# Optimization experiments

Hardware: AMD Instinct MI355X
Metric: run time of the kernel (lower is better)

Reference implementation:

```python
import jax, jax.numpy as jnp
import numpy as np

NEG_INF = -1e9
LRELU_SLOPE = 0.2  # torch GAT default leaky_relu negative slope


def setup_inputs() -> dict:
    key = jax.random.key(0)
    k1, k2, k3, k4, k5 = jax.random.split(key, 5)
    N, F_IN, H, DH = 4096, 1433, 8, 8  # n_nodes, in_features, n_heads, per-head dim (n_hidden=64)
    vert = jax.random.normal(k1, (N, F_IN), dtype=jnp.float32)
    edge = jax.random.randint(k2, (N, N), 0, 2, dtype=jnp.int32)  # dense adjacency mask
    W = jax.random.normal(k3, (F_IN, H * DH), dtype=jnp.float32) * 0.05
    a_l = jax.random.normal(k4, (H, DH), dtype=jnp.float32) * 0.05
    a_r = jax.random.normal(k5, (H, DH), dtype=jnp.float32) * 0.05
    return {"vert": vert, "edge": edge, "W": W, "a_l": a_l, "a_r": a_r}


def reference(vert, edge, W, a_l, a_r):
    # GAT-style edge-affinity layer (is_concat=True) + ELU; dropout is identity (eval mode).
    N = vert.shape[0]
    H, DH = a_l.shape
    g = (vert @ W).reshape(N, H, DH)                      # [N,H,Dh] projected node features
    sl = jnp.einsum('nhd,hd->nh', g, a_l)                 # source-node attention term
    sr = jnp.einsum('nhd,hd->nh', g, a_r)                 # target-node attention term
    e = sl[:, None, :] + sr[None, :, :]                   # [N,N,H]: attn([g_i || g_j])
    e = jnp.where(e >= 0, e, LRELU_SLOPE * e)             # leaky_relu
    mask = (edge != 0)[:, :, None]                        # [N,N,1]
    e = jnp.where(mask, e, NEG_INF)                       # mask non-edges
    a = jax.nn.softmax(e, axis=1)                         # normalize over neighbors j
    out = jnp.einsum('ijh,jhd->ihd', a, g).reshape(N, H * DH)  # aggregate + concat heads
    return jax.nn.elu(out)
```

## Files before the change

kernel.cpp:

```cpp
#include <hip/hip_runtime.h>
#include <hip/hip_bf16.h>

#define NN 4096
#define FIN 1433
#define NH 8
#define DH 8
#define HD 64
#define KP 1472
#define LOG2E 1.44269504f
#define NJS 8
#define ITB 32
#define NCHK ((NN / NJS) / 64)
#define NKS 4

typedef unsigned int u32;
typedef unsigned long long u64;
typedef float v4f __attribute__((ext_vector_type(4)));
typedef _Float16 f16;
typedef _Float16 h2 __attribute__((ext_vector_type(2)));
typedef _Float16 f16x8 __attribute__((ext_vector_type(8)));

static __device__ __forceinline__ short f2h16(float f) {
    union { f16 h; short s; } u; u.h = (f16)f; return u.s;
}
static __device__ __forceinline__ h2 u2h2(u32 x) {
    union { u32 u; h2 h; } v; v.u = x; return v.h;
}
static __device__ __forceinline__ u32 h22u(h2 x) {
    union { h2 h; u32 u; } v; v.h = x; return v.u;
}

#if __has_builtin(__builtin_amdgcn_sbfe)
#define SBFE1(x, k) __builtin_amdgcn_sbfe((int)(x), (k), 1)
#else
#define SBFE1(x, k) (((int)((x) << (31 - (k)))) >> 31)
#endif

static __device__ __forceinline__ void gload_lds16(const void* g, void* l) {
    __builtin_amdgcn_global_load_lds(
        (const __attribute__((address_space(1))) void*)g,
        (__attribute__((address_space(3))) void*)l, 16, 0, 0);
}

__global__ __launch_bounds__(256) void k_wprep(const float* __restrict__ W,
                                               short* __restrict__ Wt) {
    __shared__ float Ts[64][65];
    const int c = blockIdx.x;
    const int u = threadIdx.x;
    const int n4 = (u & 15) * 4;
    const int kr = u >> 4;
#pragma unroll
    for (int q = 0; q < 4; ++q) {
        const int kl = kr + q * 16;
        const int kg = c * 64 + kl;
        v4f v = {0.f, 0.f, 0.f, 0.f};
        if (kg < FIN) v = *(const v4f*)&W[(size_t)kg * HD + n4];
        *(v4f*)&Ts[kl][n4] = v;
    }
    __syncthreads();
    const int n = u >> 2;
    const int koff = (u & 3) * 16;
    __align__(16) short tmp[16];
#pragma unroll
    for (int r = 0; r < 16; ++r) tmp[r] = f2h16(Ts[koff + r][n]);
    *(uint4*)&Wt[(size_t)n * KP + c * 64 + koff]     = *(uint4*)&tmp[0];
    *(uint4*)&Wt[(size_t)n * KP + c * 64 + koff + 8] = *(uint4*)&tmp[8];
}

__global__ __launch_bounds__(256, 4) void k_gemm(
    const float* __restrict__ vert, const short* __restrict__ Wt,
    float* __restrict__ Cp)
{
    __shared__ float cacc[4][16][68];

    const int t = threadIdx.x, lane = t & 63, w = t >> 6;
    const int ml = lane & 15, q = lane >> 4;
    const int i0 = blockIdx.x * 16;
    const int ks = blockIdx.y;
    const float* vrow = vert + (size_t)(i0 + ml) * FIN;

    v4f acc[4];
#pragma unroll
    for (int g = 0; g < 4; ++g) acc[g] = (v4f){0.f, 0.f, 0.f, 0.f};

    for (int c = ks + 4 * w; c < 45; c += 16) {
        const int k0 = c * 32 + q * 8;
        v4f a0, a1;
        if (k0 + 7 < FIN) {
            a0 = *(const v4f*)&vrow[k0];
            a1 = *(const v4f*)&vrow[k0 + 4];
        } else {
            float tmp[8];
#pragma unroll
            for (int e = 0; e < 8; ++e)
                tmp[e] = (k0 + e < FIN) ? vrow[k0 + e] : 0.f;
            a0 = (v4f){tmp[0], tmp[1], tmp[2], tmp[3]};
            a1 = (v4f){tmp[4], tmp[5], tmp[6], tmp[7]};
        }
        const f16x8 af = {(f16)a0.x, (f16)a0.y, (f16)a0.z, (f16)a0.w,
                          (f16)a1.x, (f16)a1.y, (f16)a1.z, (f16)a1.w};
#pragma unroll
        for (int g = 0; g < 4; ++g) {
            const f16x8 bf = *(const f16x8*)&Wt[(size_t)(g * 16 + ml) * KP + k0];
            acc[g] = __builtin_amdgcn_mfma_f32_16x16x32_f16(af, bf, acc[g], 0, 0, 0);
        }
    }

#pragma unroll
    for (int g = 0; g < 4; ++g)
#pragma unroll
        for (int r = 0; r < 4; ++r)
            cacc[w][q * 4 + r][g * 16 + ml] = acc[g][r];
    __syncthreads();

    const int m = t >> 4, n4 = (t & 15) * 4;
    v4f s = (v4f){0.f, 0.f, 0.f, 0.f};
#pragma unroll
    for (int ww = 0; ww < 4; ++ww) s += *(const v4f*)&cacc[ww][m][n4];
    *(v4f*)&Cp[((size_t)ks * NN + i0 + m) * HD + n4] = s;
}

__global__ __launch_bounds__(256) void k_gpost(
    const float* __restrict__ Cp,
    const float* __restrict__ al, const float* __restrict__ ar,
    short* __restrict__ gT, short* __restrict__ eB, short* __restrict__ eD,
    float* __restrict__ Rw)
{
    const int t = threadIdx.x;
    const int gid = blockIdx.x * 256 + t;
    const int i = gid >> 4, n4 = (gid & 15) * 4;

    v4f s = (v4f){0.f, 0.f, 0.f, 0.f};
#pragma unroll
    for (int ks = 0; ks < NKS; ++ks)
        s += *(const v4f*)&Cp[((size_t)ks * NN + i) * HD + n4];

#pragma unroll
    for (int e = 0; e < 4; ++e)
        gT[(size_t)(n4 + e) * NN + i] = f2h16(s[e]);

    float pl = s.x * al[n4] + s.y * al[n4 + 1] + s.z * al[n4 + 2] + s.w * al[n4 + 3];
    float pr = s.x * ar[n4] + s.y * ar[n4 + 1] + s.z * ar[n4 + 2] + s.w * ar[n4 + 3];
    pl += __shfl_xor(pl, 1, 64);
    pr += __shfl_xor(pr, 1, 64);
    if ((t & 1) == 0) {
        const int h = (t & 15) >> 1;
        eB[h * NN + i] = f2h16(exp2f(pr * LOG2E));
        eD[h * NN + i] = f2h16(exp2f(0.2f * pr * LOG2E));
        Rw[i * NH + h] = exp2f(-0.8f * pl * LOG2E);
    }
}

__global__ __launch_bounds__(256, 4) void k_attn(
    const int* __restrict__ edge, const short* __restrict__ gT,
    const short* __restrict__ eB, const short* __restrict__ eD,
    const float* __restrict__ Rw,
    float* __restrict__ numw, float* __restrict__ denw)
{
    __shared__ __align__(16) short Gs[2][64 * 64];
    __shared__ __align__(16) short BDs[2][8 * 128];
    __shared__ __align__(16) u64 Ms[2][ITB];

    const int t = threadIdx.x, lane = t & 63, w = t >> 6;
    const int ml = lane & 15, quad = lane >> 4;
    const int m8 = ml & 7;
    const int i0 = blockIdx.x * ITB;
    const int js = blockIdx.y;
    const int jbase = js * (NN / NJS);
    const int h0 = w, h1 = w + 4;
    const bool mhi = (ml >= 8);
    const u32 one2 = 0x3C003C00u;
    const uint4 ones4 = (uint4){one2, one2, one2, one2};

    h2 Ri[2][2];
#pragma unroll
    for (int sub = 0; sub < 2; ++sub) {
        const f16 r0 = (f16)Rw[(i0 + sub * 16 + ml) * NH + h0];
        const f16 r1 = (f16)Rw[(i0 + sub * 16 + ml) * NH + h1];
        Ri[sub][0] = (h2){r0, r0};
        Ri[sub][1] = (h2){r1, r1};
    }

    const short *gsrc0, *gsrc1;
    {
        int u = t, row = u >> 3;
        gsrc0 = gT + (size_t)row * NN + jbase + (((u & 7) * 8) ^ ((row & 7) * 8));
        u = 256 + t; row = u >> 3;
        gsrc1 = gT + (size_t)row * NN + jbase + (((u & 7) * 8) ^ ((row & 7) * 8));
    }
    const short* bdsrc = nullptr;
    if (t < 128) {
        const int head = t >> 4, slot = t & 15;
        bdsrc = (slot < 8 ? eB : eD) + (size_t)head * NN + jbase + (slot & 7) * 8;
    }
    const int wub = (t & ~63) * 16;

    const int* ebase = edge + (size_t)(i0 + w * 8) * NN + jbase + lane;
    u32 er[2][8];

#define STAGE(buf, ck)                                                        \
    do {                                                                      \
        const int jc_ = (ck) * 64;                                            \
        gload_lds16(gsrc0 + jc_, (char*)Gs[buf] + wub);                       \
        gload_lds16(gsrc1 + jc_, (char*)Gs[buf] + 4096 + wub);                \
        if (t < 128) gload_lds16(bdsrc + jc_, (char*)BDs[buf] + wub);         \
    } while (0)

#define ELOAD(bank, ck)                                                       \
    do {                                                                      \
        const int jo_ = (ck) * 64;                                            \
        _Pragma("unroll")                                                     \
        for (int rr = 0; rr < 8; ++rr)                                        \
            er[bank][rr] = __builtin_nontemporal_load(ebase + (size_t)rr * NN + jo_); \
    } while (0)

#define EBALLOT(buf, bank)                                                    \
    do {                                                                      \
        _Pragma("unroll")                                                     \
        for (int rr = 0; rr < 8; ++rr) {                                      \
            const u64 b_ = __ballot(er[bank][rr] != 0);                       \
            if (lane == 0) Ms[buf][w * 8 + rr] = b_;                          \
        }                                                                     \
    } while (0)

    v4f acc[2][2];
#pragma unroll
    for (int sub = 0; sub < 2; ++sub) {
        acc[sub][0] = (v4f){0.f, 0.f, 0.f, 0.f};
        acc[sub][1] = (v4f){0.f, 0.f, 0.f, 0.f};
    }

    STAGE(0, 0);
    ELOAD(0, 0);
    EBALLOT(0, 0);
    ELOAD(1, 1);

    for (int c = 0; c < NCHK; ++c) {
        const int cb = c & 1, nb = cb ^ 1;
        __syncthreads();
        const bool pf = (c + 1) < NCHK;
        if (pf) STAGE(nb, c + 1);
        if (c + 2 < NCHK) ELOAD(cb, c + 2);

        union { u64 q; uint2 d; } m0u, m1u;
        m0u.q = Ms[cb][ml];
        m1u.q = Ms[cb][16 + ml];

#pragma unroll
        for (int s = 0; s < 2; ++s) {
            const int xj = s * 32 + quad * 8;
            const int xg = xj ^ (m8 * 8);
            union { uint4 u; f16x8 h; } g0u, g1u;
            g0u.u = mhi ? ones4 : *(const uint4*)&Gs[cb][(h0 * 8 + m8) * 64 + xg];
            g1u.u = mhi ? ones4 : *(const uint4*)&Gs[cb][(h1 * 8 + m8) * 64 + xg];
            const uint4 bu0 = *(const uint4*)&BDs[cb][h0 * 128 + xj];
            const uint4 du0 = *(const uint4*)&BDs[cb][h0 * 128 + 64 + xj];
            const uint4 bu1 = *(const uint4*)&BDs[cb][h1 * 128 + xj];
            const uint4 du1 = *(const uint4*)&BDs[cb][h1 * 128 + 64 + xj];
#pragma unroll
            for (int sub = 0; sub < 2; ++sub) {
                const u32 half = sub ? ((s ? m1u.d.y : m1u.d.x))
                                     : ((s ? m0u.d.y : m0u.d.x));
                const u32 w8 = half >> (quad * 8);
                u32 m[4];
#pragma unroll
                for (int k = 0; k < 4; ++k) {
                    const int ea = SBFE1(w8, 2 * k);
                    const int eb = SBFE1(w8, 2 * k + 1);
                    m[k] = __builtin_amdgcn_perm((u32)eb, (u32)ea, 0x05040100u);
                }
                u32 aw0[4], aw1[4];
#pragma unroll
                for (int k = 0; k < 4; ++k) {
                    const u32 rd0 = h22u(Ri[sub][0] * u2h2((&du0.x)[k]));
                    const u32 rd1 = h22u(Ri[sub][1] * u2h2((&du1.x)[k]));
                    u32 p0, p1;
                    asm("v_pk_max_f16 %0, %1, %2" : "=v"(p0) : "v"(rd0), "v"((&bu0.x)[k]));
                    asm("v_pk_max_f16 %0, %1, %2" : "=v"(p1) : "v"(rd1), "v"((&bu1.x)[k]));
                    aw0[k] = p0 & m[k];
                    aw1[k] = p1 & m[k];
                }
                union { uint4 u; f16x8 h; } a0u, a1u;
                a0u.u = (uint4){aw0[0], aw0[1], aw0[2], aw0[3]};
                a1u.u = (uint4){aw1[0], aw1[1], aw1[2], aw1[3]};
                acc[sub][0] = __builtin_amdgcn_mfma_f32_16x16x32_f16(
                    a0u.h, g0u.h, acc[sub][0], 0, 0, 0);
                acc[sub][1] = __builtin_amdgcn_mfma_f32_16x16x32_f16(
                    a1u.h, g1u.h, acc[sub][1], 0, 0, 0);
            }
        }
        if (pf) EBALLOT(nb, nb);
    }
#undef STAGE
#undef ELOAD
#undef EBALLOT

    float* nw = numw + (size_t)js * NN * HD;
    float* dw = denw + (size_t)js * NN * NH;
#pragma unroll
    for (int sub = 0; sub < 2; ++sub) {
        const int ibase = i0 + sub * 16 + quad * 4;
#pragma unroll
        for (int hh = 0; hh < 2; ++hh) {
            const int h = w + hh * 4;
#pragma unroll
            for (int r = 0; r < 4; ++r) {
                if (ml < 8)       nw[(ibase + r) * HD + h * 8 + ml] = acc[sub][hh][r];
                else if (ml == 8) dw[(ibase + r) * NH + h]          = acc[sub][hh][r];
            }
        }
    }
}

__global__ __launch_bounds__(256) void k_comb(
    const float* __restrict__ numw, const float* __restrict__ denw,
    float* __restrict__ out)
{
    const int gid = blockIdx.x * 256 + threadIdx.x;
    const int i = gid >> 6, h = (gid & 63) >> 3;
    float num = 0.f, den = 0.f;
#pragma unroll
    for (int s = 0; s < NJS; ++s) {
        num += numw[(size_t)s * NN * HD + gid];
        den += denw[(size_t)s * NN * NH + i * NH + h];
    }
    float x = num / den;
    out[gid] = (x > 0.f) ? x : (__expf(x) - 1.f);
}

extern "C" void kernel_launch(void* const* d_in, const int* in_sizes, int n_in,
                              void* d_out, int out_size, void* d_ws, size_t ws_size,
                              hipStream_t stream) {
    const float* vert = (const float*)d_in[0];
    const int*   edge = (const int*)d_in[1];
    const float* W    = (const float*)d_in[2];
    const float* al   = (const float*)d_in[3];
    const float* ar   = (const float*)d_in[4];
    float* out = (float*)d_out;

    char* ws = (char*)d_ws;
    short* gT    = (short*)ws;
    short* eB    = (short*)(ws + 512 * 1024);
    short* eD    = (short*)(ws + 576 * 1024);
    float* Rw    = (float*)(ws + 640 * 1024);
    short* Wt    = (short*)(ws + 768 * 1024);
    float* Cp    = (float*)(ws + 3 * 1024 * 1024);
    float* numw  = (float*)(ws + 7 * 1024 * 1024);
    float* denw  = (float*)(ws + 15 * 1024 * 1024);

    hipLaunchKernelGGL(k_wprep, dim3(23), dim3(256), 0, stream, W, Wt);
    hipLaunchKernelGGL(k_gemm, dim3(NN / 16, NKS), dim3(256), 0, stream,
                       vert, Wt, Cp);
    hipLaunchKernelGGL(k_gpost, dim3(NN * 16 / 256), dim3(256), 0, stream,
                       Cp, al, ar, gT, eB, eD, Rw);
    hipLaunchKernelGGL(k_attn, dim3(NN / ITB, NJS), dim3(256), 0, stream,
                       edge, gT, eB, eD, Rw, numw, denw);
    hipLaunchKernelGGL(k_comb, dim3(NN * HD / 256), dim3(256), 0, stream,
                       numw, denw, out);
}
```

Before: 150.4 us.

## Restructure attention kernel: per-wave 16 rows across all heads, whole-segment LDS staging

Each wave now owns 16 destination rows and computes all 8 heads, instead of the block splitting heads across waves. The full 256-column j-segment of projected features is staged into LDS once up front, and the chunked double-buffered pipeline becomes a short unrolled sequence of edge loads, ballots and MFMA compute. The eB/eD exponent tables are read straight from global memory rather than through LDS, and the j-dimension split doubles to 16. The aim is to cut per-chunk barriers and LDS staging overhead and to raise parallelism. In exchange it adds larger partial-sum buffers for the combine kernel, a larger LDS footprint and more register pressure from holding 8 head accumulators.

```diff
diff --git a/kernel.cpp b/kernel.cpp
--- a/kernel.cpp
+++ b/kernel.cpp
@@ -8,9 +8,9 @@
 #define HD 64
 #define KP 1472
 #define LOG2E 1.44269504f
-#define NJS 8
-#define ITB 32
-#define NCHK ((NN / NJS) / 64)
+#define NJS 16
+#define JSEG (NN / NJS)
+#define NCHK (JSEG / 64)
 #define NKS 4
 
 typedef unsigned int u32;
@@ -157,157 +157,126 @@
     const float* __restrict__ Rw,
     float* __restrict__ numw, float* __restrict__ denw)
 {
-    __shared__ __align__(16) short Gs[2][64 * 64];
-    __shared__ __align__(16) short BDs[2][8 * 128];
-    __shared__ __align__(16) u64 Ms[2][ITB];
+    __shared__ __align__(16) short Gs[64 * JSEG];
+    __shared__ u64 Msw[4][16];
 
     const int t = threadIdx.x, lane = t & 63, w = t >> 6;
     const int ml = lane & 15, quad = lane >> 4;
     const int m8 = ml & 7;
-    const int i0 = blockIdx.x * ITB;
+    const int i0w = blockIdx.x * 64 + w * 16;
     const int js = blockIdx.y;
-    const int jbase = js * (NN / NJS);
-    const int h0 = w, h1 = w + 4;
+    const int jbase = js * JSEG;
     const bool mhi = (ml >= 8);
     const u32 one2 = 0x3C003C00u;
     const uint4 ones4 = (uint4){one2, one2, one2, one2};
 
-    h2 Ri[2][2];
-#pragma unroll
-    for (int sub = 0; sub < 2; ++sub) {
-        const f16 r0 = (f16)Rw[(i0 + sub * 16 + ml) * NH + h0];
-        const f16 r1 = (f16)Rw[(i0 + sub * 16 + ml) * NH + h1];
-        Ri[sub][0] = (h2){r0, r0};
-        Ri[sub][1] = (h2){r1, r1};
-    }
-
-    const short *gsrc0, *gsrc1;
+    h2 Ri[8];
     {
-        int u = t, row = u >> 3;
-        gsrc0 = gT + (size_t)row * NN + jbase + (((u & 7) * 8) ^ ((row & 7) * 8));
-        u = 256 + t; row = u >> 3;
-        gsrc1 = gT + (size_t)row * NN + jbase + (((u & 7) * 8) ^ ((row & 7) * 8));
-    }
-    const short* bdsrc = nullptr;
-    if (t < 128) {
-        const int head = t >> 4, slot = t & 15;
-        bdsrc = (slot < 8 ? eB : eD) + (size_t)head * NN + jbase + (slot & 7) * 8;
-    }
-    const int wub = (t & ~63) * 16;
-
-    const int* ebase = edge + (size_t)(i0 + w * 8) * NN + jbase + lane;
-    u32 er[2][8];
-
-#define STAGE(buf, ck)                                                        \
-    do {                                                                      \
-        const int jc_ = (ck) * 64;                                            \
-        gload_lds16(gsrc0 + jc_, (char*)Gs[buf] + wub);                       \
-        gload_lds16(gsrc1 + jc_, (char*)Gs[buf] + 4096 + wub);                \
-        if (t < 128) gload_lds16(bdsrc + jc_, (char*)BDs[buf] + wub);         \
-    } while (0)
+        const v4f rlo = *(const v4f*)&Rw[(size_t)(i0w + ml) * NH];
+        const v4f rhi = *(const v4f*)&Rw[(size_t)(i0w + ml) * NH + 4];
+#pragma unroll
+        for (int h = 0; h < 4; ++h) {
+            const f16 a = (f16)rlo[h], b = (f16)rhi[h];
+            Ri[h]     = (h2){a, a};
+            Ri[h + 4] = (h2){b, b};
+        }
+    }
+
+#pragma unroll
+    for (int r8 = 0; r8 < 8; ++r8) {
+        const int u = r8 * 256 + t;
+        const int row = u >> 5, c16 = u & 31;
+        const int col = (c16 * 8) ^ ((row & 7) * 8);
+        gload_lds16(gT + (size_t)row * NN + jbase + col,
+                    (char*)Gs + r8 * 4096 + (t & ~63) * 16);
+    }
+
+    const short* eBj = eB + jbase;
+    const short* eDj = eD + jbase;
+    const int* ebase = edge + (size_t)i0w * NN + jbase + lane;
+
+    u32 erA[16], erB[16];
 
 #define ELOAD(bank, ck)                                                       \
     do {                                                                      \
-        const int jo_ = (ck) * 64;                                            \
         _Pragma("unroll")                                                     \
-        for (int rr = 0; rr < 8; ++rr)                                        \
-            er[bank][rr] = __builtin_nontemporal_load(ebase + (size_t)rr * NN + jo_); \
+        for (int rr = 0; rr < 16; ++rr)                                       \
+            bank[rr] = __builtin_nontemporal_load(                            \
+                ebase + (size_t)rr * NN + (ck) * 64);                         \
     } while (0)
 
-#define EBALLOT(buf, bank)                                                    \
+#define EBAL(bank)                                                            \
     do {                                                                      \
         _Pragma("unroll")                                                     \
-        for (int rr = 0; rr < 8; ++rr) {                                      \
-            const u64 b_ = __ballot(er[bank][rr] != 0);                       \
-            if (lane == 0) Ms[buf][w * 8 + rr] = b_;                          \
+        for (int rr = 0; rr < 16; ++rr) {                                     \
+            const u64 b_ = __ballot(bank[rr] != 0);                           \
+            if (lane == 0) Msw[w][rr] = b_;                                   \
         }                                                                     \
     } while (0)
 
-    v4f acc[2][2];
-#pragma unroll
-    for (int sub = 0; sub < 2; ++sub) {
-        acc[sub][0] = (v4f){0.f, 0.f, 0.f, 0.f};
-        acc[sub][1] = (v4f){0.f, 0.f, 0.f, 0.f};
-    }
-
-    STAGE(0, 0);
-    ELOAD(0, 0);
-    EBALLOT(0, 0);
-    ELOAD(1, 1);
-
-    for (int c = 0; c < NCHK; ++c) {
-        const int cb = c & 1, nb = cb ^ 1;
-        __syncthreads();
-        const bool pf = (c + 1) < NCHK;
-        if (pf) STAGE(nb, c + 1);
-        if (c + 2 < NCHK) ELOAD(cb, c + 2);
-
-        union { u64 q; uint2 d; } m0u, m1u;
-        m0u.q = Ms[cb][ml];
-        m1u.q = Ms[cb][16 + ml];
-
-#pragma unroll
-        for (int s = 0; s < 2; ++s) {
-            const int xj = s * 32 + quad * 8;
-            const int xg = xj ^ (m8 * 8);
-            union { uint4 u; f16x8 h; } g0u, g1u;
-            g0u.u = mhi ? ones4 : *(const uint4*)&Gs[cb][(h0 * 8 + m8) * 64 + xg];
-            g1u.u = mhi ? ones4 : *(const uint4*)&Gs[cb][(h1 * 8 + m8) * 64 + xg];
-            const uint4 bu0 = *(const uint4*)&BDs[cb][h0 * 128 + xj];
-            const uint4 du0 = *(const uint4*)&BDs[cb][h0 * 128 + 64 + xj];
-            const uint4 bu1 = *(const uint4*)&BDs[cb][h1 * 128 + xj];
-            const uint4 du1 = *(const uint4*)&BDs[cb][h1 * 128 + 64 + xj];
-#pragma unroll
-            for (int sub = 0; sub < 2; ++sub) {
-                const u32 half = sub ? ((s ? m1u.d.y : m1u.d.x))
-                                     : ((s ? m0u.d.y : m0u.d.x));
-                const u32 w8 = half >> (quad * 8);
-                u32 m[4];
-#pragma unroll
-                for (int k = 0; k < 4; ++k) {
-                    const int ea = SBFE1(w8, 2 * k);
-                    const int eb = SBFE1(w8, 2 * k + 1);
-                    m[k] = __builtin_amdgcn_perm((u32)eb, (u32)ea, 0x05040100u);
-                }
-                u32 aw0[4], aw1[4];
-#pragma unroll
-                for (int k = 0; k < 4; ++k) {
-                    const u32 rd0 = h22u(Ri[sub][0] * u2h2((&du0.x)[k]));
-                    const u32 rd1 = h22u(Ri[sub][1] * u2h2((&du1.x)[k]));
-                    u32 p0, p1;
-                    asm("v_pk_max_f16 %0, %1, %2" : "=v"(p0) : "v"(rd0), "v"((&bu0.x)[k]));
-                    asm("v_pk_max_f16 %0, %1, %2" : "=v"(p1) : "v"(rd1), "v"((&bu1.x)[k]));
-                    aw0[k] = p0 & m[k];
-                    aw1[k] = p1 & m[k];
-                }
-                union { uint4 u; f16x8 h; } a0u, a1u;
-                a0u.u = (uint4){aw0[0], aw0[1], aw0[2], aw0[3]};
-                a1u.u = (uint4){aw1[0], aw1[1], aw1[2], aw1[3]};
-                acc[sub][0] = __builtin_amdgcn_mfma_f32_16x16x32_f16(
-                    a0u.h, g0u.h, acc[sub][0], 0, 0, 0);
-                acc[sub][1] = __builtin_amdgcn_mfma_f32_16x16x32_f16(
-                    a1u.h, g1u.h, acc[sub][1], 0, 0, 0);
-            }
-        }
-        if (pf) EBALLOT(nb, nb);
-    }
-#undef STAGE
+#define COMPUTE(ck)                                                           \
+    do {                                                                      \
+        const u64 mask64 = Msw[w][ml];                                        \
+        _Pragma("unroll")                                                     \
+        for (int s = 0; s < 2; ++s) {                                         \
+            const int jj = (ck) * 64 + s * 32 + quad * 8;                     \
+            const u32 w8 = (u32)(mask64 >> (s * 32 + quad * 8));              \
+            u32 m[4];                                                         \
+            _Pragma("unroll")                                                 \
+            for (int k = 0; k < 4; ++k) {                                     \
+                const int ea = SBFE1(w8, 2 * k);                              \
+                const int eb = SBFE1(w8, 2 * k + 1);                          \
+                m[k] = __builtin_amdgcn_perm((u32)eb, (u32)ea, 0x05040100u);  \
+            }                                                                 \
+            const int xg = jj ^ (m8 * 8);                                     \
+            _Pragma("unroll")                                                 \
+            for (int h = 0; h < 8; ++h) {                                     \
+                const uint4 gu = *(const uint4*)&Gs[(h * 8 + m8) * JSEG + xg];\
+                const uint4 bu = *(const uint4*)&eBj[(size_t)h * NN + jj];    \
+                const uint4 du = *(const uint4*)&eDj[(size_t)h * NN + jj];    \
+                u32 aw[4];                                                    \
+                _Pragma("unroll")                                             \
+                for (int k = 0; k < 4; ++k) {                                 \
+                    const u32 rd = h22u(Ri[h] * u2h2((&du.x)[k]));            \
+                    u32 p;                                                    \
+                    asm("v_pk_max_f16 %0, %1, %2"                             \
+                        : "=v"(p) : "v"(rd), "v"((&bu.x)[k]));                \
+                    aw[k] = p & m[k];                                         \
+                }                                                             \
+                union { uint4 u; f16x8 h; } au, gv;                           \
+                au.u = (uint4){aw[0], aw[1], aw[2], aw[3]};                   \
+                gv.u = mhi ? ones4 : gu;                                      \
+                acc[h] = __builtin_amdgcn_mfma_f32_16x16x32_f16(              \
+                    au.h, gv.h, acc[h], 0, 0, 0);                             \
+            }                                                                 \
+        }                                                                     \
+    } while (0)
+
+    v4f acc[8];
+#pragma unroll
+    for (int h = 0; h < 8; ++h) acc[h] = (v4f){0.f, 0.f, 0.f, 0.f};
+
+    ELOAD(erA, 0);
+    __syncthreads();
+
+    ELOAD(erB, 1); EBAL(erA); COMPUTE(0);
+    ELOAD(erA, 2); EBAL(erB); COMPUTE(1);
+    ELOAD(erB, 3); EBAL(erA); COMPUTE(2);
+                   EBAL(erB); COMPUTE(3);
+
 #undef ELOAD
-#undef EBALLOT
+#undef EBAL
+#undef COMPUTE
 
     float* nw = numw + (size_t)js * NN * HD;
     float* dw = denw + (size_t)js * NN * NH;
-#pragma unroll
-    for (int sub = 0; sub < 2; ++sub) {
-        const int ibase = i0 + sub * 16 + quad * 4;
-#pragma unroll
-        for (int hh = 0; hh < 2; ++hh) {
-            const int h = w + hh * 4;
-#pragma unroll
-            for (int r = 0; r < 4; ++r) {
-                if (ml < 8)       nw[(ibase + r) * HD + h * 8 + ml] = acc[sub][hh][r];
-                else if (ml == 8) dw[(ibase + r) * NH + h]          = acc[sub][hh][r];
-            }
+    const int ibase = i0w + quad * 4;
+#pragma unroll
+    for (int h = 0; h < 8; ++h) {
+#pragma unroll
+        for (int r = 0; r < 4; ++r) {
+            if (ml < 8)       nw[(size_t)(ibase + r) * HD + h * 8 + ml] = acc[h][r];
+            else if (ml == 8) dw[(size_t)(ibase + r) * NH + h]          = acc[h][r];
         }
     }
 }
@@ -344,16 +313,16 @@
     short* eD    = (short*)(ws + 576 * 1024);
     float* Rw    = (float*)(ws + 640 * 1024);
     short* Wt    = (short*)(ws + 768 * 1024);
-    float* Cp    = (float*)(ws + 3 * 1024 * 1024);
-    float* numw  = (float*)(ws + 7 * 1024 * 1024);
-    float* denw  = (float*)(ws + 15 * 1024 * 1024);
+    float* Cp    = (float*)(ws + 1024 * 1024);
+    float* numw  = (float*)(ws + 5 * 1024 * 1024);
+    float* denw  = (float*)(ws + 21 * 1024 * 1024);
 
     hipLaunchKernelGGL(k_wprep, dim3(23), dim3(256), 0, stream, W, Wt);
     hipLaunchKernelGGL(k_gemm, dim3(NN / 16, NKS), dim3(256), 0, stream,
                        vert, Wt, Cp);
     hipLaunchKernelGGL(k_gpost, dim3(NN * 16 / 256), dim3(256), 0, stream,
                        Cp, al, ar, gT, eB, eD, Rw);
-    hipLaunchKernelGGL(k_attn, dim3(NN / ITB, NJS), dim3(256), 0, stream,
+    hipLaunchKernelGGL(k_attn, dim3(NN / 64, NJS), dim3(256), 0, stream,
                        edge, gT, eB, eD, Rw, numw, denw);
     hipLaunchKernelGGL(k_comb, dim3(NN * HD / 256), dim3(256), 0, stream,
                        numw, denw, out);
```

Result: slower. 166.1 us (+10.4%).

## Preload all edge-mask chunks into shared memory before the main loop

Applied to the files above, without the earlier changes.

Instead of streaming edge-mask loads two chunks ahead and balloting inside the main loop, each block now loads all eight chunks of its edge rows up front, keeping four 8-register banks in flight, and stores every ballot mask in a per-chunk shared array. The main loop then only does staging and MFMA work. This aims to take global edge-load latency out of the steady-state loop and raise memory-level parallelism on the dominant int32 adjacency read. The cost is a serialized prologue before any compute can start, plus extra registers and shared memory, which could reduce overlap of edge loads with MFMA work.

```diff
diff --git a/kernel.cpp b/kernel.cpp
--- a/kernel.cpp
+++ b/kernel.cpp
@@ -159,7 +159,7 @@
 {
     __shared__ __align__(16) short Gs[2][64 * 64];
     __shared__ __align__(16) short BDs[2][8 * 128];
-    __shared__ __align__(16) u64 Ms[2][ITB];
+    __shared__ __align__(16) u64 Ms[NCHK][ITB];
 
     const int t = threadIdx.x, lane = t & 63, w = t >> 6;
     const int ml = lane & 15, quad = lane >> 4;
@@ -196,7 +196,6 @@
     const int wub = (t & ~63) * 16;
 
     const int* ebase = edge + (size_t)(i0 + w * 8) * NN + jbase + lane;
-    u32 er[2][8];
 
 #define STAGE(buf, ck)                                                        \
     do {                                                                      \
@@ -206,20 +205,20 @@
         if (t < 128) gload_lds16(bdsrc + jc_, (char*)BDs[buf] + wub);         \
     } while (0)
 
-#define ELOAD(bank, ck)                                                       \
+#define ELOADB(bank, ck)                                                      \
     do {                                                                      \
-        const int jo_ = (ck) * 64;                                            \
         _Pragma("unroll")                                                     \
         for (int rr = 0; rr < 8; ++rr)                                        \
-            er[bank][rr] = __builtin_nontemporal_load(ebase + (size_t)rr * NN + jo_); \
+            bank[rr] = __builtin_nontemporal_load(                            \
+                ebase + (size_t)rr * NN + (ck) * 64);                         \
     } while (0)
 
-#define EBALLOT(buf, bank)                                                    \
+#define EBALB(bank, ck)                                                       \
     do {                                                                      \
         _Pragma("unroll")                                                     \
         for (int rr = 0; rr < 8; ++rr) {                                      \
-            const u64 b_ = __ballot(er[bank][rr] != 0);                       \
-            if (lane == 0) Ms[buf][w * 8 + rr] = b_;                          \
+            const u64 b_ = __ballot(bank[rr] != 0);                           \
+            if (lane == 0) Ms[ck][w * 8 + rr] = b_;                           \
         }                                                                     \
     } while (0)
 
@@ -231,20 +230,25 @@
     }
 
     STAGE(0, 0);
-    ELOAD(0, 0);
-    EBALLOT(0, 0);
-    ELOAD(1, 1);
+    {
+        u32 eb0[8], eb1[8], eb2[8], eb3[8];
+        ELOADB(eb0, 0); ELOADB(eb1, 1); ELOADB(eb2, 2); ELOADB(eb3, 3);
+        EBALB(eb0, 0);  ELOADB(eb0, 4);
+        EBALB(eb1, 1);  ELOADB(eb1, 5);
+        EBALB(eb2, 2);  ELOADB(eb2, 6);
+        EBALB(eb3, 3);  ELOADB(eb3, 7);
+        EBALB(eb0, 4);  EBALB(eb1, 5);  EBALB(eb2, 6);  EBALB(eb3, 7);
+    }
+    __syncthreads();
 
     for (int c = 0; c < NCHK; ++c) {
         const int cb = c & 1, nb = cb ^ 1;
-        __syncthreads();
         const bool pf = (c + 1) < NCHK;
         if (pf) STAGE(nb, c + 1);
-        if (c + 2 < NCHK) ELOAD(cb, c + 2);
 
         union { u64 q; uint2 d; } m0u, m1u;
-        m0u.q = Ms[cb][ml];
-        m1u.q = Ms[cb][16 + ml];
+        m0u.q = Ms[c][ml];
+        m1u.q = Ms[c][16 + ml];
 
 #pragma unroll
         for (int s = 0; s < 2; ++s) {
@@ -289,11 +293,11 @@
                     a1u.h, g1u.h, acc[sub][1], 0, 0, 0);
             }
         }
-        if (pf) EBALLOT(nb, nb);
+        __syncthreads();
     }
 #undef STAGE
-#undef ELOAD
-#undef EBALLOT
+#undef ELOADB
+#undef EBALB
 
     float* nw = numw + (size_t)js * NN * HD;
     float* dw = denw + (size_t)js * NN * NH;
```

Measured after the change: 153.0 us. About the same (+1.7%).
